# Optimization experiments

Measured on AMD Instinct MI355X. Metric: run time of the kernel, lower is better.

## Reference

```python
import jax, jax.numpy as jnp
import numpy as np

N, D, C = 8192, 128, 64
LAMBDA = 0.25
DELTA = 1.0


def setup_inputs() -> dict:
    key = jax.random.key(0)
    k1, k2, k3 = jax.random.split(key, 3)
    out = jax.random.normal(k1, (N, C), dtype=jnp.float32)
    feat = jax.random.normal(k2, (N, D), dtype=jnp.float32)
    y = jax.random.randint(k3, (N,), 0, C)
    return {"out": out, "feat": feat, "y": y}


def reference(out, feat, y):
    n = feat.shape[0]
    # Per-class matrices: zeroing rows not in class c leaves singular values
    # identical to slicing X[y==c] (extra zero rows only add zero singular
    # directions), so one batched SVD over [C, N, D] replaces the CPU loop.
    masks = (y[None, :] == jnp.arange(C)[:, None]).astype(feat.dtype)  # [C, N]
    Xc = feat[None, :, :] * masks[:, :, None]                           # [C, N, D]
    Sc = jnp.linalg.svd(Xc, compute_uv=False)                           # [C, min(N,D)]
    obj_c = jnp.maximum(Sc.sum(-1), DELTA).sum()                        # sum_c max(||X_c||_*, DELTA)
    S_all = jnp.linalg.svd(feat, compute_uv=False)
    ole = (obj_c - S_all.sum()) / n * LAMBDA
    # Cross entropy (mean reduction, matching nn.CrossEntropyLoss)
    logp = jax.nn.log_softmax(out, axis=-1)
    xe = -jnp.take_along_axis(logp, y[:, None], axis=1).mean()
    loss = ole + xe
    return jnp.reshape(loss, (1,))  # torch returns shape-[1] tensor
```

## Files before the change

### kernel.cpp

```cpp
#include <hip/hip_runtime.h>
#include <math.h>


#define N_ROWS 8192
#define DIM    128
#define NCLS   64
#define NB_CE  64
#define NB_BLD 16
#define NITER  6
#define EPSN   2e-4f
#define LAMBDA_ 0.25f
#define DELTA_  1.0f
#define MAGIC  0x13579BDF

typedef __attribute__((ext_vector_type(8))) short s16x8;
typedef __attribute__((ext_vector_type(4))) short s16x4;
typedef __attribute__((ext_vector_type(4))) float f32x4;

static __device__ const float NS_C1[NITER] =
  {2.554408f, 2.491084f, 2.189178f, 2.050122f, 1.686417f, 1.5f};
static __device__ const float NS_C2[NITER] =
  {2.469261f, 2.290137f, 1.554316f, 1.276543f, 0.710544f, 0.5f};

__device__ __forceinline__ unsigned short f2bf(float f) {
  unsigned u = __float_as_uint(f);
  u = (u + 0x7FFFu + ((u >> 16) & 1u)) >> 16;
  return (unsigned short)u;
}
__device__ __forceinline__ float bf2f(unsigned short h) {
  return __uint_as_float(((unsigned)h) << 16);
}

__device__ __forceinline__ int swz_idx(int i, int j) {
  return i * 128 + (((j >> 3) ^ (i & 15)) << 3) + (j & 7);
}

__device__ __forceinline__ s16x8 load_frag(const short* buf, int row0,
                                           int kstep, int lane) {
  int m  = row0 + (lane & 15);
  int kg = kstep * 4 + (lane >> 4);
  return *(const s16x8*)(buf + m * 128 + ((kg ^ (m & 15)) << 3));
}

__device__ __forceinline__ void flag_set(int* p) {
  __threadfence();
  __hip_atomic_store(p, MAGIC, __ATOMIC_RELEASE, __HIP_MEMORY_SCOPE_AGENT);
}
__device__ __forceinline__ void flag_wait(const int* p) {
  while (__hip_atomic_load(p, __ATOMIC_ACQUIRE, __HIP_MEMORY_SCOPE_AGENT) != MAGIC)
    __builtin_amdgcn_s_sleep(8);
}

__global__ __launch_bounds__(512, 1) void ole_fused(const float* __restrict__ feat,
                                                    const int* __restrict__ y,
                                                    const float* __restrict__ logits,
                                                    float* __restrict__ G,
                                                    float* __restrict__ nuc,
                                                    float* __restrict__ cepart,
                                                    int* __restrict__ flags,
                                                    float* __restrict__ out) {
  int* gramdone = flags;
  int* gallf    = flags + 64;
  int* nflag    = flags + 80;
  int* ceflag   = flags + 144;

  __shared__ __align__(16) short Yb[DIM * DIM];
  __shared__ __align__(16) short Db[DIM * DIM];
  __shared__ __align__(16) short Zb[DIM * DIM];
  __shared__ int cnt;

  const int bid  = blockIdx.x;
  const int tid  = threadIdx.x;
  const int lane = tid & 63;
  const int quad = lane >> 4;
  const int wv   = tid >> 6;

  float* Gall = G + (size_t)NCLS * DIM * DIM;

  if (bid > NCLS && bid <= NCLS + NB_CE) {
    const int gwave = (bid - NCLS - 1) * 8 + wv;
    float acc = 0.f;
    for (int row = gwave; row < N_ROWS; row += 512) {
      float v = logits[row * NCLS + lane];
      float mx = v;
      for (int off = 32; off > 0; off >>= 1) mx = fmaxf(mx, __shfl_xor(mx, off, 64));
      float e = expf(v - mx);
      for (int off = 32; off > 0; off >>= 1) e += __shfl_xor(e, off, 64);
      if (lane == 0) {
        int t = y[row];
        acc += (mx + logf(e)) - logits[row * NCLS + t];
      }
    }
    if (lane == 0) cepart[gwave] = acc;
    __syncthreads();
    if (tid == 0) flag_set(&ceflag[bid - NCLS - 1]);
    return;
  }

  if (bid > NCLS + NB_CE) {
    const int gb = bid - (NCLS + 1 + NB_CE);
    if (tid < NCLS) flag_wait(&gramdone[tid]);
    __syncthreads();
    if (tid < 256) {
      const int idx4 = gb * 256 + tid;
      const float4* G4 = (const float4*)G;
      float4 s = make_float4(0.f, 0.f, 0.f, 0.f);
#pragma unroll 8
      for (int c = 0; c < NCLS; ++c) {
        float4 v = G4[(size_t)c * (DIM * DIM / 4) + idx4];
        s.x += v.x; s.y += v.y; s.z += v.z; s.w += v.w;
      }
      ((float4*)Gall)[idx4] = s;
    }
    __syncthreads();
    if (tid == 0) flag_set(&gallf[gb]);
    return;
  }

  const int ti = tid >> 5, tj = tid & 31;
  const int i0 = ti * 8,  j0 = tj * 4;

  float tpart = 0.f, fpart = 0.f;
  float4 gs[8];
  float  accg[8][4];

  if (bid < NCLS) {
    int* list = (int*)Yb;
    if (tid == 0) cnt = 0;
    __syncthreads();
#pragma unroll
    for (int t = 0; t < 16; ++t) {
      int row = t * 512 + tid;
      bool hit = (y[row] == bid);
      unsigned long long m = __ballot(hit);
      int base = 0;
      if (lane == 0 && m) base = atomicAdd(&cnt, __popcll(m));
      base = __shfl(base, 0, 64);
      if (hit) {
        int pre = __popcll(m & ((1ull << lane) - 1ull));
        list[base + pre] = row;
      }
    }
    __syncthreads();
    const int n = cnt;

    float (*xs)[DIM] = (float (*)[DIM])Db;

#pragma unroll
    for (int a = 0; a < 8; ++a)
#pragma unroll
      for (int b = 0; b < 4; ++b) accg[a][b] = 0.f;

    {
      float4 v = make_float4(0.f, 0.f, 0.f, 0.f);
      if (ti < n) v = *(const float4*)(feat + (size_t)list[ti] * DIM + j0);
      *(float4*)(&xs[ti][j0]) = v;
    }
    __syncthreads();

    int buf = 0;
    for (int base = 0; base < n; base += 16, buf ^= 1) {
      int li = base + 16 + ti;
      float4 vn = make_float4(0.f, 0.f, 0.f, 0.f);
      if (li < n) vn = *(const float4*)(feat + (size_t)list[li] * DIM + j0);
#pragma unroll
      for (int rw = 0; rw < 16; ++rw) {
        float xi[8], xj[4];
#pragma unroll
        for (int a = 0; a < 8; ++a) xi[a] = xs[buf * 16 + rw][i0 + a];
#pragma unroll
        for (int b = 0; b < 4; ++b) xj[b] = xs[buf * 16 + rw][j0 + b];
#pragma unroll
        for (int a = 0; a < 8; ++a)
#pragma unroll
          for (int b = 0; b < 4; ++b) accg[a][b] = fmaf(xi[a], xj[b], accg[a][b]);
      }
      *(float4*)(&xs[(buf ^ 1) * 16 + ti][j0]) = vn;
      __syncthreads();
    }

    float* Gc = G + (size_t)bid * DIM * DIM;
#pragma unroll
    for (int a = 0; a < 8; ++a) {
      float4 row;
      float* rp = (float*)&row;
#pragma unroll
      for (int b = 0; b < 4; ++b) {
        float g = accg[a][b];
        rp[b] = g;
        fpart += g * g;
        if (i0 + a == j0 + b) tpart += g;
      }
      *(float4*)(Gc + (size_t)(i0 + a) * DIM + j0) = row;
    }
    __syncthreads();
    if (tid == 0) flag_set(&gramdone[bid]);
  } else {
    if (tid < NB_BLD) flag_wait(&gallf[tid]);
    __syncthreads();
    const float4* Gm4 = (const float4*)Gall;
#pragma unroll
    for (int t = 0; t < 8; ++t) {
      int idx4 = tid + 512 * t;
      float4 v = Gm4[idx4];
      gs[t] = v;
      fpart += v.x * v.x + v.y * v.y + v.z * v.z + v.w * v.w;
      int flat = idx4 * 4, i = flat >> 7, jj = flat & 127;
      if (jj <= i && i < jj + 4) tpart += ((const float*)&v)[i - jj];
    }
  }

  for (int off = 32; off > 0; off >>= 1) {
    tpart += __shfl_down(tpart, off, 64);
    fpart += __shfl_down(fpart, off, 64);
  }
  float* redf = (float*)Zb;
  if (lane == 0) { redf[wv] = tpart; redf[8 + wv] = fpart; }
  __syncthreads();
  float trace = 0.f, fro2 = 0.f;
#pragma unroll
  for (int w = 0; w < 8; ++w) { trace += redf[w]; fro2 += redf[8 + w]; }
  __syncthreads();

  float s = sqrtf(fro2);
  if (s < 1e-12f) s = 1.f;
  const float invs = 1.f / s;
  const float eps  = EPSN * trace * invs;

  if (bid < NCLS) {
#pragma unroll
    for (int a = 0; a < 8; ++a) {
      int i = i0 + a;
      s16x4 vh;
#pragma unroll
      for (int b = 0; b < 4; ++b) {
        float x = accg[a][b] * invs + ((i == j0 + b) ? eps : 0.f);
        vh[b] = (short)f2bf(x);
      }
      *(s16x4*)(Yb + swz_idx(i, j0)) = vh;
    }
  } else {
#pragma unroll
    for (int t = 0; t < 8; ++t) {
      int idx4 = tid + 512 * t;
      int flat = idx4 * 4, i = flat >> 7, jj = flat & 127;
      s16x4 vh;
#pragma unroll
      for (int e = 0; e < 4; ++e) {
        float x = ((const float*)&gs[t])[e] * invs + ((i == jj + e) ? eps : 0.f);
        vh[e] = (short)f2bf(x);
      }
      *(s16x4*)(Yb + swz_idx(i, jj)) = vh;
    }
  }
  for (int grp = tid; grp < DIM * 16; grp += 512) {
    int i = grp >> 4, g = grp & 15;
    s16x8 v = (s16x8)0;
    if ((i >> 3) == g) v[i & 7] = (short)0x3F80;
    *(s16x8*)(Zb + i * 128 + ((g ^ (i & 15)) << 3)) = v;
  }
  __syncthreads();

  const int wr = wv >> 2;
  const int wc = wv & 3;

  for (int it = 0; it < NITER - 1; ++it) {
    const float kA = NS_C1[it];
    const float kB = NS_C2[it];

    f32x4 acc[4][2];
#pragma unroll
    for (int r = 0; r < 4; ++r)
#pragma unroll
      for (int c2 = 0; c2 < 2; ++c2) acc[r][c2] = (f32x4)0.f;
#pragma unroll
    for (int ks = 0; ks < 4; ++ks) {
      s16x8 a[4], b[2];
#pragma unroll
      for (int r = 0; r < 4; ++r) a[r] = load_frag(Zb, (4 * wr + r) * 16, ks, lane);
#pragma unroll
      for (int c2 = 0; c2 < 2; ++c2) b[c2] = load_frag(Yb, (2 * wc + c2) * 16, ks, lane);
#pragma unroll
      for (int r = 0; r < 4; ++r)
#pragma unroll
        for (int c2 = 0; c2 < 2; ++c2)
          acc[r][c2] = __builtin_amdgcn_mfma_f32_16x16x32_bf16(a[r], b[c2], acc[r][c2], 0, 0, 0);
    }
#pragma unroll
    for (int r = 0; r < 4; ++r) {
      int ibase = (4 * wr + r) * 16 + quad * 4;
      int cg    = ibase >> 3;
#pragma unroll
      for (int c2 = 0; c2 < 2; ++c2) {
        int jg  = (2 * wc + c2) * 16 + (lane & 15);
        int idx = jg * 128 + ((cg ^ (jg & 15)) << 3) + (ibase & 7);
        s16x4 vd;
#pragma unroll
        for (int e = 0; e < 4; ++e) {
          float dv = -kB * acc[r][c2][e] + ((ibase + e == jg) ? (kA - 1.f) : 0.f);
          dv = fminf(fmaxf(dv, -4.f), 4.f);
          vd[e] = (short)f2bf(dv);
        }
        *(s16x4*)(Db + idx) = vd;
      }
    }
    __syncthreads();

    f32x4 ay[4][2], az[4][2];
#pragma unroll
    for (int r = 0; r < 4; ++r) {
      int ibase = (4 * wr + r) * 16 + quad * 4;
      int cg    = ibase >> 3;
#pragma unroll
      for (int c2 = 0; c2 < 2; ++c2) {
        int jg  = (2 * wc + c2) * 16 + (lane & 15);
        int idx = jg * 128 + ((cg ^ (jg & 15)) << 3) + (ibase & 7);
        s16x4 yv = *(const s16x4*)(Yb + idx);
        s16x4 zv = *(const s16x4*)(Zb + idx);
#pragma unroll
        for (int e = 0; e < 4; ++e) {
          ay[r][c2][e] = bf2f((unsigned short)yv[e]);
          az[r][c2][e] = bf2f((unsigned short)zv[e]);
        }
      }
    }
#pragma unroll
    for (int ks = 0; ks < 4; ++ks) {
      s16x8 aD[4], bY[2], bZ[2];
#pragma unroll
      for (int r = 0; r < 4; ++r)
        aD[r] = load_frag(Db, (4 * wr + r) * 16, ks, lane);
#pragma unroll
      for (int c2 = 0; c2 < 2; ++c2) {
        int cb = (2 * wc + c2) * 16;
        bY[c2] = load_frag(Yb, cb, ks, lane);
        bZ[c2] = load_frag(Zb, cb, ks, lane);
      }
#pragma unroll
      for (int r = 0; r < 4; ++r)
#pragma unroll
        for (int c2 = 0; c2 < 2; ++c2) {
          ay[r][c2] = __builtin_amdgcn_mfma_f32_16x16x32_bf16(aD[r], bY[c2], ay[r][c2], 0, 0, 0);
          az[r][c2] = __builtin_amdgcn_mfma_f32_16x16x32_bf16(aD[r], bZ[c2], az[r][c2], 0, 0, 0);
        }
    }
    __syncthreads();

#pragma unroll
    for (int r = 0; r < 4; ++r) {
      int ibase = (4 * wr + r) * 16 + quad * 4;
      int cg    = ibase >> 3;
#pragma unroll
      for (int c2 = 0; c2 < 2; ++c2) {
        int jg  = (2 * wc + c2) * 16 + (lane & 15);
        int idx = jg * 128 + ((cg ^ (jg & 15)) << 3) + (ibase & 7);
        s16x4 vy, vz;
#pragma unroll
        for (int e = 0; e < 4; ++e) {
          vy[e] = (short)f2bf(ay[r][c2][e]);
          vz[e] = (short)f2bf(az[r][c2][e]);
        }
        *(s16x4*)(Yb + idx) = vy;
        *(s16x4*)(Zb + idx) = vz;
      }
    }
    __syncthreads();
  }

  {
    const float kA = NS_C1[NITER - 1];
    const float kB = NS_C2[NITER - 1];

    f32x4 acc[4][2];
#pragma unroll
    for (int r = 0; r < 4; ++r)
#pragma unroll
      for (int c2 = 0; c2 < 2; ++c2) acc[r][c2] = (f32x4)0.f;
#pragma unroll
    for (int ks = 0; ks < 4; ++ks) {
      s16x8 a[4], b[2];
#pragma unroll
      for (int r = 0; r < 4; ++r) a[r] = load_frag(Zb, (4 * wr + r) * 16, ks, lane);
#pragma unroll
      for (int c2 = 0; c2 < 2; ++c2) b[c2] = load_frag(Yb, (2 * wc + c2) * 16, ks, lane);
#pragma unroll
      for (int r = 0; r < 4; ++r)
#pragma unroll
        for (int c2 = 0; c2 < 2; ++c2)
          acc[r][c2] = __builtin_amdgcn_mfma_f32_16x16x32_bf16(a[r], b[c2], acc[r][c2], 0, 0, 0);
    }
#pragma unroll
    for (int r = 0; r < 4; ++r) {
      int ibase = (4 * wr + r) * 16 + quad * 4;
      int cg    = ibase >> 3;
#pragma unroll
      for (int c2 = 0; c2 < 2; ++c2) {
        int jg  = (2 * wc + c2) * 16 + (lane & 15);
        int idx = jg * 128 + ((cg ^ (jg & 15)) << 3) + (ibase & 7);
        s16x4 vd;
#pragma unroll
        for (int e = 0; e < 4; ++e) {
          float dv = -kB * acc[r][c2][e] + ((ibase + e == jg) ? (kA - 1.f) : 0.f);
          dv = fminf(fmaxf(dv, -4.f), 4.f);
          vd[e] = (short)f2bf(dv);
        }
        *(s16x4*)(Db + idx) = vd;
      }
    }
    __syncthreads();

    f32x4 az[4][2];
#pragma unroll
    for (int r = 0; r < 4; ++r) {
      int ibase = (4 * wr + r) * 16 + quad * 4;
      int cg    = ibase >> 3;
#pragma unroll
      for (int c2 = 0; c2 < 2; ++c2) {
        int jg  = (2 * wc + c2) * 16 + (lane & 15);
        int idx = jg * 128 + ((cg ^ (jg & 15)) << 3) + (ibase & 7);
        s16x4 zv = *(const s16x4*)(Zb + idx);
#pragma unroll
        for (int e = 0; e < 4; ++e) az[r][c2][e] = bf2f((unsigned short)zv[e]);
      }
    }
#pragma unroll
    for (int ks = 0; ks < 4; ++ks) {
      s16x8 aD[4], bZ[2];
#pragma unroll
      for (int r = 0; r < 4; ++r)
        aD[r] = load_frag(Db, (4 * wr + r) * 16, ks, lane);
#pragma unroll
      for (int c2 = 0; c2 < 2; ++c2)
        bZ[c2] = load_frag(Zb, (2 * wc + c2) * 16, ks, lane);
#pragma unroll
      for (int r = 0; r < 4; ++r)
#pragma unroll
        for (int c2 = 0; c2 < 2; ++c2)
          az[r][c2] = __builtin_amdgcn_mfma_f32_16x16x32_bf16(aD[r], bZ[c2], az[r][c2], 0, 0, 0);
    }
    __syncthreads();

#pragma unroll
    for (int r = 0; r < 4; ++r) {
      int ibase = (4 * wr + r) * 16 + quad * 4;
      int cg    = ibase >> 3;
#pragma unroll
      for (int c2 = 0; c2 < 2; ++c2) {
        int jg  = (2 * wc + c2) * 16 + (lane & 15);
        int idx = jg * 128 + ((cg ^ (jg & 15)) << 3) + (ibase & 7);
        s16x4 vz;
#pragma unroll
        for (int e = 0; e < 4; ++e) vz[e] = (short)f2bf(az[r][c2][e]);
        *(s16x4*)(Zb + idx) = vz;
      }
    }
    __syncthreads();
  }

  float t_gz = 0.f, t_z = 0.f, t_z3 = 0.f;
  if (bid < NCLS) {
#pragma unroll
    for (int a = 0; a < 8; ++a) {
      s16x4 zv = *(const s16x4*)(Zb + swz_idx(i0 + a, j0));
#pragma unroll
      for (int b = 0; b < 4; ++b) t_gz += accg[a][b] * bf2f((unsigned short)zv[b]);
    }
  } else {
#pragma unroll
    for (int t = 0; t < 8; ++t) {
      int idx4 = tid + 512 * t;
      int flat = idx4 * 4, i = flat >> 7, jj = flat & 127;
      s16x4 zv = *(const s16x4*)(Zb + swz_idx(i, jj));
#pragma unroll
      for (int e = 0; e < 4; ++e) t_gz += ((const float*)&gs[t])[e] * bf2f((unsigned short)zv[e]);
    }
  }
  if (tid < DIM) t_z = bf2f((unsigned short)Zb[swz_idx(tid, tid)]);

  {
    f32x4 u[4][2];
#pragma unroll
    for (int r = 0; r < 4; ++r)
#pragma unroll
      for (int c2 = 0; c2 < 2; ++c2) u[r][c2] = (f32x4)0.f;
#pragma unroll
    for (int ks = 0; ks < 4; ++ks) {
      s16x8 a[4], b[2];
#pragma unroll
      for (int r = 0; r < 4; ++r) a[r] = load_frag(Zb, (4 * wr + r) * 16, ks, lane);
#pragma unroll
      for (int c2 = 0; c2 < 2; ++c2) b[c2] = load_frag(Zb, (2 * wc + c2) * 16, ks, lane);
#pragma unroll
      for (int r = 0; r < 4; ++r)
#pragma unroll
        for (int c2 = 0; c2 < 2; ++c2)
          u[r][c2] = __builtin_amdgcn_mfma_f32_16x16x32_bf16(a[r], b[c2], u[r][c2], 0, 0, 0);
    }
#pragma unroll
    for (int r = 0; r < 4; ++r) {
      int ibase = (4 * wr + r) * 16 + quad * 4;
      int cg    = ibase >> 3;
#pragma unroll
      for (int c2 = 0; c2 < 2; ++c2) {
        int jg  = (2 * wc + c2) * 16 + (lane & 15);
        int idx = jg * 128 + ((cg ^ (jg & 15)) << 3) + (ibase & 7);
        s16x4 zt = *(const s16x4*)(Zb + idx);
#pragma unroll
        for (int e = 0; e < 4; ++e) t_z3 += u[r][c2][e] * bf2f((unsigned short)zt[e]);
      }
    }
  }

  for (int off = 32; off > 0; off >>= 1) {
    t_gz += __shfl_down(t_gz, off, 64);
    t_z  += __shfl_down(t_z,  off, 64);
    t_z3 += __shfl_down(t_z3, off, 64);
  }
  __syncthreads();
  float* red = (float*)Db;
  if (lane == 0) { red[wv] = t_gz; red[8 + wv] = t_z; red[16 + wv] = t_z3; }
  __syncthreads();

  float nuc_own = 0.f;
  if (tid == 0) {
    float gz = 0.f, z1 = 0.f, z3 = 0.f;
#pragma unroll
    for (int w = 0; w < 8; ++w) { gz += red[w]; z1 += red[8 + w]; z3 += red[16 + w]; }
    float trsq = gz * invs + 0.5f * eps * z1 - 0.125f * eps * eps * z3;
    nuc_own = sqrtf(s) * trsq;
    nuc[bid] = nuc_own;
  }

  if (bid < NCLS) {
    if (tid == 0) flag_set(&nflag[bid]);
    return;
  }

  if (tid < NCLS)          flag_wait(&nflag[tid]);
  else if (tid < 2 * NCLS) flag_wait(&ceflag[tid - NCLS]);
  __syncthreads();

  float ce2 = cepart[tid];
  float vmx = (tid < NCLS) ? fmaxf(nuc[tid], DELTA_) : 0.f;
  for (int off = 32; off > 0; off >>= 1) {
    vmx += __shfl_down(vmx, off, 64);
    ce2 += __shfl_down(ce2, off, 64);
  }
  if (lane == 0) { red[wv] = vmx; red[8 + wv] = ce2; }
  __syncthreads();
  if (tid == 0) {
    float vs = 0.f, cs = 0.f;
#pragma unroll
    for (int w = 0; w < 8; ++w) { vs += red[w]; cs += red[8 + w]; }
    float ole = (vs - nuc_own) * (LAMBDA_ / (float)N_ROWS);
    out[0] = ole + cs / (float)N_ROWS;
  }
}

extern "C" void kernel_launch(void* const* d_in, const int* in_sizes, int n_in,
                              void* d_out, int out_size, void* d_ws, size_t ws_size,
                              hipStream_t stream) {
  const float* logits = (const float*)d_in[0];
  const float* feat   = (const float*)d_in[1];
  const int*   yp     = (const int*)d_in[2];

  int*   flags  = (int*)d_ws;
  float* nuc    = (float*)d_ws + 256;
  float* cepart = nuc + 68;
  float* G      = cepart + 512;

  hipMemsetAsync(d_ws, 0, 256 * sizeof(int), stream);

  ole_fused<<<NCLS + 1 + NB_CE + NB_BLD, 512, 0, stream>>>(
      feat, yp, logits, G, nuc, cepart, flags, (float*)d_out);
}
```

Before: 120.7 us.

## Compute global Gram directly from feat rows with atomic accumulation

Previously the full-matrix Gram was built by summing the 64 per-class Gram matrices, which first had to be written to global memory, with each block waiting on all class blocks to finish. Now 96 extra blocks each compute a partial Gram over about 85 rows of feat and atomically add it into a zeroed Gall buffer. This removes the 64 per-class Gram stores, the dependency on class blocks, and the 64x reduction reads. In exchange it adds 128x128 float atomics per block, a larger memset, and non-deterministic summation order.

After: 124.3 us. 1.03x slower.

```diff
diff --git a/kernel.cpp b/kernel.cpp
--- a/kernel.cpp
+++ b/kernel.cpp
@@ -6,7 +6,7 @@
 #define DIM    128
 #define NCLS   64
 #define NB_CE  64
-#define NB_BLD 16
+#define NB_GALL 96
 #define NITER  6
 #define EPSN   2e-4f
 #define LAMBDA_ 0.25f
@@ -54,15 +54,14 @@
 __global__ __launch_bounds__(512, 1) void ole_fused(const float* __restrict__ feat,
                                                     const int* __restrict__ y,
                                                     const float* __restrict__ logits,
-                                                    float* __restrict__ G,
+                                                    float* __restrict__ Gall,
                                                     float* __restrict__ nuc,
                                                     float* __restrict__ cepart,
                                                     int* __restrict__ flags,
                                                     float* __restrict__ out) {
-  int* gramdone = flags;
-  int* gallf    = flags + 64;
-  int* nflag    = flags + 80;
-  int* ceflag   = flags + 144;
+  int* gallf  = flags;
+  int* nflag  = flags + 96;
+  int* ceflag = flags + 160;
 
   __shared__ __align__(16) short Yb[DIM * DIM];
   __shared__ __align__(16) short Db[DIM * DIM];
@@ -74,8 +73,6 @@
   const int lane = tid & 63;
   const int quad = lane >> 4;
   const int wv   = tid >> 6;
-
-  float* Gall = G + (size_t)NCLS * DIM * DIM;
 
   if (bid > NCLS && bid <= NCLS + NB_CE) {
     const int gwave = (bid - NCLS - 1) * 8 + wv;
@@ -99,19 +96,50 @@
 
   if (bid > NCLS + NB_CE) {
     const int gb = bid - (NCLS + 1 + NB_CE);
-    if (tid < NCLS) flag_wait(&gramdone[tid]);
-    __syncthreads();
-    if (tid < 256) {
-      const int idx4 = gb * 256 + tid;
-      const float4* G4 = (const float4*)G;
-      float4 s = make_float4(0.f, 0.f, 0.f, 0.f);
-#pragma unroll 8
-      for (int c = 0; c < NCLS; ++c) {
-        float4 v = G4[(size_t)c * (DIM * DIM / 4) + idx4];
-        s.x += v.x; s.y += v.y; s.z += v.z; s.w += v.w;
-      }
-      ((float4*)Gall)[idx4] = s;
-    }
+    const int rbase = gb * 85 + (gb < 32 ? gb : 32);
+    const int n = (gb < 32) ? 86 : 85;
+    const int ti = tid >> 5, tj = tid & 31;
+    const int i0 = ti * 8, j0 = tj * 4;
+
+    float ag[8][4];
+#pragma unroll
+    for (int a = 0; a < 8; ++a)
+#pragma unroll
+      for (int b = 0; b < 4; ++b) ag[a][b] = 0.f;
+
+    float (*xs)[DIM] = (float (*)[DIM])Db;
+    {
+      float4 v = make_float4(0.f, 0.f, 0.f, 0.f);
+      if (ti < n) v = *(const float4*)(feat + (size_t)(rbase + ti) * DIM + j0);
+      *(float4*)(&xs[ti][j0]) = v;
+    }
+    __syncthreads();
+    int buf = 0;
+    for (int base = 0; base < n; base += 16, buf ^= 1) {
+      int li = base + 16 + ti;
+      float4 vn = make_float4(0.f, 0.f, 0.f, 0.f);
+      if (li < n) vn = *(const float4*)(feat + (size_t)(rbase + li) * DIM + j0);
+#pragma unroll
+      for (int rw = 0; rw < 16; ++rw) {
+        float xi[8], xj[4];
+#pragma unroll
+        for (int a = 0; a < 8; ++a) xi[a] = xs[buf * 16 + rw][i0 + a];
+#pragma unroll
+        for (int b = 0; b < 4; ++b) xj[b] = xs[buf * 16 + rw][j0 + b];
+#pragma unroll
+        for (int a = 0; a < 8; ++a)
+#pragma unroll
+          for (int b = 0; b < 4; ++b) ag[a][b] = fmaf(xi[a], xj[b], ag[a][b]);
+      }
+      *(float4*)(&xs[(buf ^ 1) * 16 + ti][j0]) = vn;
+      __syncthreads();
+    }
+
+#pragma unroll
+    for (int a = 0; a < 8; ++a)
+#pragma unroll
+      for (int b = 0; b < 4; ++b)
+        atomicAdd(&Gall[(i0 + a) * DIM + (j0 + b)], ag[a][b]);
     __syncthreads();
     if (tid == 0) flag_set(&gallf[gb]);
     return;
@@ -179,24 +207,16 @@
       __syncthreads();
     }
 
-    float* Gc = G + (size_t)bid * DIM * DIM;
-#pragma unroll
-    for (int a = 0; a < 8; ++a) {
-      float4 row;
-      float* rp = (float*)&row;
+#pragma unroll
+    for (int a = 0; a < 8; ++a)
 #pragma unroll
       for (int b = 0; b < 4; ++b) {
         float g = accg[a][b];
-        rp[b] = g;
         fpart += g * g;
         if (i0 + a == j0 + b) tpart += g;
       }
-      *(float4*)(Gc + (size_t)(i0 + a) * DIM + j0) = row;
-    }
-    __syncthreads();
-    if (tid == 0) flag_set(&gramdone[bid]);
   } else {
-    if (tid < NB_BLD) flag_wait(&gallf[tid]);
+    if (tid < NB_GALL) flag_wait(&gallf[tid]);
     __syncthreads();
     const float4* Gm4 = (const float4*)Gall;
 #pragma unroll
@@ -564,13 +584,13 @@
   const float* feat   = (const float*)d_in[1];
   const int*   yp     = (const int*)d_in[2];
 
-  int*   flags  = (int*)d_ws;
-  float* nuc    = (float*)d_ws + 256;
+  float* Gall   = (float*)d_ws;
+  int*   flags  = (int*)(Gall + DIM * DIM);
+  float* nuc    = (float*)(flags + 256);
   float* cepart = nuc + 68;
-  float* G      = cepart + 512;
-
-  hipMemsetAsync(d_ws, 0, 256 * sizeof(int), stream);
-
-  ole_fused<<<NCLS + 1 + NB_CE + NB_BLD, 512, 0, stream>>>(
-      feat, yp, logits, G, nuc, cepart, flags, (float*)d_out);
-}
+
+  hipMemsetAsync(d_ws, 0, (DIM * DIM + 256) * sizeof(float), stream);
+
+  ole_fused<<<NCLS + 1 + NB_CE + NB_GALL, 512, 0, stream>>>(
+      feat, yp, logits, Gall, nuc, cepart, flags, (float*)d_out);
+}
```

## Accumulate class Gram matrices into global sum via atomics, drop reduction blocks

Applied to the files above, without the earlier changes.

Each class block now atomically adds its 128x128 Gram matrix into a single shared Gall buffer instead of writing a per-class copy that 16 separate reduction blocks later summed. This removes the extra reduction stage, its flag handoff and the 64x64KB intermediate writes and reads, and the total-Gram consumer now waits directly on the per-class flags. In exchange there are 64x16384 float atomic adds on the same addresses, which may contend, and the summation order becomes nondeterministic. The memset grows to clear Gall each call.

After: 126.7 us. 5.0% more time.

```diff
diff --git a/kernel.cpp b/kernel.cpp
--- a/kernel.cpp
+++ b/kernel.cpp
@@ -6,7 +6,6 @@
 #define DIM    128
 #define NCLS   64
 #define NB_CE  64
-#define NB_BLD 16
 #define NITER  6
 #define EPSN   2e-4f
 #define LAMBDA_ 0.25f
@@ -54,15 +53,14 @@
 __global__ __launch_bounds__(512, 1) void ole_fused(const float* __restrict__ feat,
                                                     const int* __restrict__ y,
                                                     const float* __restrict__ logits,
-                                                    float* __restrict__ G,
+                                                    float* __restrict__ Gall,
                                                     float* __restrict__ nuc,
                                                     float* __restrict__ cepart,
                                                     int* __restrict__ flags,
                                                     float* __restrict__ out) {
   int* gramdone = flags;
-  int* gallf    = flags + 64;
-  int* nflag    = flags + 80;
-  int* ceflag   = flags + 144;
+  int* nflag    = flags + 64;
+  int* ceflag   = flags + 128;
 
   __shared__ __align__(16) short Yb[DIM * DIM];
   __shared__ __align__(16) short Db[DIM * DIM];
@@ -75,9 +73,7 @@
   const int quad = lane >> 4;
   const int wv   = tid >> 6;
 
-  float* Gall = G + (size_t)NCLS * DIM * DIM;
-
-  if (bid > NCLS && bid <= NCLS + NB_CE) {
+  if (bid > NCLS) {
     const int gwave = (bid - NCLS - 1) * 8 + wv;
     float acc = 0.f;
     for (int row = gwave; row < N_ROWS; row += 512) {
@@ -97,26 +93,6 @@
     return;
   }
 
-  if (bid > NCLS + NB_CE) {
-    const int gb = bid - (NCLS + 1 + NB_CE);
-    if (tid < NCLS) flag_wait(&gramdone[tid]);
-    __syncthreads();
-    if (tid < 256) {
-      const int idx4 = gb * 256 + tid;
-      const float4* G4 = (const float4*)G;
-      float4 s = make_float4(0.f, 0.f, 0.f, 0.f);
-#pragma unroll 8
-      for (int c = 0; c < NCLS; ++c) {
-        float4 v = G4[(size_t)c * (DIM * DIM / 4) + idx4];
-        s.x += v.x; s.y += v.y; s.z += v.z; s.w += v.w;
-      }
-      ((float4*)Gall)[idx4] = s;
-    }
-    __syncthreads();
-    if (tid == 0) flag_set(&gallf[gb]);
-    return;
-  }
-
   const int ti = tid >> 5, tj = tid & 31;
   const int i0 = ti * 8,  j0 = tj * 4;
 
@@ -179,24 +155,19 @@
       __syncthreads();
     }
 
-    float* Gc = G + (size_t)bid * DIM * DIM;
-#pragma unroll
-    for (int a = 0; a < 8; ++a) {
-      float4 row;
-      float* rp = (float*)&row;
+#pragma unroll
+    for (int a = 0; a < 8; ++a)
 #pragma unroll
       for (int b = 0; b < 4; ++b) {
         float g = accg[a][b];
-        rp[b] = g;
         fpart += g * g;
         if (i0 + a == j0 + b) tpart += g;
-      }
-      *(float4*)(Gc + (size_t)(i0 + a) * DIM + j0) = row;
-    }
+        atomicAdd(&Gall[(i0 + a) * DIM + (j0 + b)], g);
+      }
     __syncthreads();
     if (tid == 0) flag_set(&gramdone[bid]);
   } else {
-    if (tid < NB_BLD) flag_wait(&gallf[tid]);
+    if (tid < NCLS) flag_wait(&gramdone[tid]);
     __syncthreads();
     const float4* Gm4 = (const float4*)Gall;
 #pragma unroll
@@ -564,13 +535,13 @@
   const float* feat   = (const float*)d_in[1];
   const int*   yp     = (const int*)d_in[2];
 
-  int*   flags  = (int*)d_ws;
-  float* nuc    = (float*)d_ws + 256;
+  float* Gall   = (float*)d_ws;
+  int*   flags  = (int*)(Gall + DIM * DIM);
+  float* nuc    = (float*)(flags + 256);
   float* cepart = nuc + 68;
-  float* G      = cepart + 512;
-
-  hipMemsetAsync(d_ws, 0, 256 * sizeof(int), stream);
-
-  ole_fused<<<NCLS + 1 + NB_CE + NB_BLD, 512, 0, stream>>>(
-      feat, yp, logits, G, nuc, cepart, flags, (float*)d_out);
-}
+
+  hipMemsetAsync(d_ws, 0, (DIM * DIM + 256) * sizeof(float), stream);
+
+  ole_fused<<<NCLS + 1 + NB_CE, 512, 0, stream>>>(
+      feat, yp, logits, Gall, nuc, cepart, flags, (float*)d_out);
+}
```
